# Kernel optimization log

Hardware: AMD Instinct MI355X
Metric: run time of the kernel (lower is better)

Reference implementation:

```python
import jax, jax.numpy as jnp
import numpy as np

IN_SZ = 256
OUT_SZ = 256
RANK = 60  # min(60, IN_SZ*OUT_SZ)
C = 512    # channel_size
N_SEL = 256
B = 1024


def setup_inputs() -> dict:
    key = jax.random.key(0)
    k_x, k_u, k_v, k_b, k_i = jax.random.split(key, 5)
    # match torch init scales: U ~ U(-sqrt(3/rank), ...), V ~ U(-sqrt(1/(in*out)),...)
    bu = np.sqrt(3.0 / RANK)
    bv = np.sqrt(1.0 / (IN_SZ * OUT_SZ))
    bb = np.sqrt(1.0 / RANK)
    x = jax.random.normal(k_x, (N_SEL, B, IN_SZ), dtype=jnp.float32)
    weights_U = jax.random.uniform(k_u, (C, RANK), jnp.float32, -bu, bu)
    weights_V = jax.random.uniform(k_v, (RANK, IN_SZ * OUT_SZ), jnp.float32, -bv, bv)
    bias = jax.random.uniform(k_b, (C, 1, OUT_SZ), jnp.float32, -bb, bb)
    indices = jax.random.randint(k_i, (N_SEL,), 0, C, dtype=jnp.int64)
    return {"x": x, "indices": indices, "weights_U": weights_U,
            "weights_V": weights_V, "bias": bias}


def reference(x, indices, weights_U, weights_V, bias):
    # Synthesize full per-channel weights, then gather selected channels
    # (faithful to the original: full U @ V materialized before gather).
    weight = (weights_U @ weights_V).reshape(-1, IN_SZ, OUT_SZ)  # [C, in, out]
    w = weight[indices]                                          # [n, in, out]
    # per-channel batched matmul: [n, B, in] x [n, in, out] -> [n, B, out]
    out = jnp.einsum('nbi,nio->nbo', x, w) + bias[indices]
    return out
```

## Files before the change

### kernel.cpp

```cpp
#include <hip/hip_runtime.h>
#include <hip/hip_bf16.h>
#include <stdint.h>

#define IN_SZ   256
#define OUT_SZ  256
#define RANK    60
#define NSEL    256
#define BATCH   1024
#define WELEMS  (IN_SZ * OUT_SZ)

typedef __attribute__((ext_vector_type(8))) short          short8;
typedef __attribute__((ext_vector_type(4))) float          f32x4;
typedef __attribute__((ext_vector_type(4))) unsigned short u16x4;

static __device__ __forceinline__ unsigned short f32_to_bf16(float f) {
    union { float f; uint32_t u; } c; c.f = f;
    uint32_t u = c.u;
    u += 0x7fffu + ((u >> 16) & 1u);
    return (unsigned short)(u >> 16);
}

__global__ __launch_bounds__(256) void synth_w(
    const float* __restrict__ U, const float* __restrict__ V,
    const int* __restrict__ idx, unsigned short* __restrict__ wt)
{
    __shared__ unsigned short Cs[16][2064];

    int bid = blockIdx.x;
    int L   = (bid & 7) * 64 + (bid >> 3);
    int ic  = L >> 4;
    int g16 = L & 15;

    int tid = threadIdx.x, lane = tid & 63, wv = tid >> 6;

    int arow = lane & 15;
    int c    = idx[g16 * 16 + arow];
    short8 afr[2];
    #pragma unroll
    for (int ks = 0; ks < 2; ++ks) {
        short8 h;
        #pragma unroll
        for (int j = 0; j < 8; ++j) {
            int r = ks * 32 + (lane >> 4) * 8 + j;
            float u = (r < RANK) ? U[c * RANK + r] : 0.f;
            h[j] = (short)f32_to_bf16(u);
        }
        afr[ks] = h;
    }

    const float* Vb = V + (size_t)ic * 2048;
    #pragma unroll 2
    for (int mt = 0; mt < 32; ++mt) {
        int mloc = (wv * 32 + mt) * 16 + (lane & 15);
        f32x4 acc = {};
        #pragma unroll
        for (int ks = 0; ks < 2; ++ks) {
            short8 b;
            #pragma unroll
            for (int j = 0; j < 8; ++j) {
                int r = ks * 32 + (lane >> 4) * 8 + j;
                float v = (r < RANK) ? Vb[(size_t)r * WELEMS + mloc] : 0.f;
                b[j] = (short)f32_to_bf16(v);
            }
            acc = __builtin_amdgcn_mfma_f32_16x16x32_bf16(afr[ks], b, acc, 0, 0, 0);
        }
        #pragma unroll
        for (int j = 0; j < 4; ++j) {
            int nl = (lane >> 4) * 4 + j;
            Cs[nl][wv * 512 + mt * 16 + (lane & 15)] = f32_to_bf16(acc[j]);
        }
    }
    __syncthreads();

    #pragma unroll
    for (int t0 = 0; t0 < 16; ++t0) {
        int t  = t0 * 256 + tid;
        int nl = t >> 8;
        int o  = t & 255;
        short8 h;
        #pragma unroll
        for (int il = 0; il < 8; ++il) h[il] = (short)Cs[nl][il * 256 + o];
        int n = g16 * 16 + nl;
        size_t base = (size_t)n * WELEMS + (size_t)ic * 2048 + (size_t)o * 8;
        *reinterpret_cast<short8*>(wt + base) = h;
    }
}

__global__ __launch_bounds__(256, 3) void gemm_k(
    const float* __restrict__ x, const int* __restrict__ idx,
    const unsigned short* __restrict__ wt, const float* __restrict__ bias,
    float* __restrict__ out)
{
    __shared__ __align__(16) unsigned short As[64 * 256];

    int bid = blockIdx.x;
    int L   = (bid & 7) * 512 + (bid >> 3);
    int n   = L >> 4;
    int mt  = L & 15;

    int tid  = threadIdx.x;
    int lane = tid & 63;
    int wv   = tid >> 6;
    int r16  = lane & 15;
    int q    = lane >> 4;

    const float*          xn = x  + (size_t)n * (BATCH * IN_SZ) + (size_t)mt * 64 * IN_SZ;
    const unsigned short* wb = wt + (size_t)n * WELEMS;

    #pragma unroll
    for (int p = 0; p < 8; ++p) {
        int id    = p * 256 + tid;
        int row   = id >> 5;
        int chunk = id & 31;
        const float* gp = xn + (size_t)row * IN_SZ + chunk * 8;
        float4 v0 = *reinterpret_cast<const float4*>(gp);
        float4 v1 = *reinterpret_cast<const float4*>(gp + 4);
        short8 h;
        h[0] = (short)f32_to_bf16(v0.x); h[1] = (short)f32_to_bf16(v0.y);
        h[2] = (short)f32_to_bf16(v0.z); h[3] = (short)f32_to_bf16(v0.w);
        h[4] = (short)f32_to_bf16(v1.x); h[5] = (short)f32_to_bf16(v1.y);
        h[6] = (short)f32_to_bf16(v1.z); h[7] = (short)f32_to_bf16(v1.w);
        int off = row * 512 + ((chunk * 16) ^ ((row & 7) << 4));
        *reinterpret_cast<short8*>(&As[off >> 1]) = h;
    }
    __syncthreads();

    f32x4 acc[4][4] = {};

    #pragma unroll
    for (int ks = 0; ks < 8; ++ks) {
        short8 af[4], bf[4];
        #pragma unroll
        for (int mf = 0; mf < 4; ++mf) {
            int row = mf * 16 + r16;
            int off = row * 512 + ((ks * 64 + q * 16) ^ ((row & 7) << 4));
            af[mf] = *reinterpret_cast<const short8*>(&As[off >> 1]);
        }
        #pragma unroll
        for (int nf = 0; nf < 4; ++nf) {
            int o = wv * 64 + nf * 16 + r16;
            bf[nf] = *reinterpret_cast<const short8*>(
                wb + (size_t)((ks * 4 + q) * 2048 + o * 8));
        }
        #pragma unroll
        for (int mf = 0; mf < 4; ++mf)
            #pragma unroll
            for (int nf = 0; nf < 4; ++nf)
                acc[mf][nf] = __builtin_amdgcn_mfma_f32_16x16x32_bf16(
                    af[mf], bf[nf], acc[mf][nf], 0, 0, 0);
    }

    int c = idx[n];
    float bv[4];
    #pragma unroll
    for (int nf = 0; nf < 4; ++nf)
        bv[nf] = bias[(size_t)c * OUT_SZ + wv * 64 + nf * 16 + r16];

    float* on = out + (size_t)n * (BATCH * OUT_SZ) + (size_t)mt * 64 * OUT_SZ;
    #pragma unroll
    for (int mf = 0; mf < 4; ++mf) {
        int r0 = mf * 16 + q * 4;
        #pragma unroll
        for (int nf = 0; nf < 4; ++nf) {
            int o = wv * 64 + nf * 16 + r16;
            #pragma unroll
            for (int j = 0; j < 4; ++j)
                on[(size_t)(r0 + j) * OUT_SZ + o] = acc[mf][nf][j] + bv[nf];
        }
    }
}

extern "C" void kernel_launch(void* const* d_in, const int* in_sizes, int n_in,
                              void* d_out, int out_size, void* d_ws, size_t ws_size,
                              hipStream_t stream) {
    const float* x    = (const float*)d_in[0];
    const int*   idx  = (const int*)  d_in[1];
    const float* U    = (const float*)d_in[2];
    const float* V    = (const float*)d_in[3];
    const float* bias = (const float*)d_in[4];
    float* out = (float*)d_out;
    unsigned short* wt = (unsigned short*)d_ws;
    (void)in_sizes; (void)n_in; (void)out_size; (void)ws_size;

    synth_w<<<dim3(512),  dim3(256), 0, stream>>>(U, V, idx, wt);
    gemm_k <<<dim3(4096), dim3(256), 0, stream>>>(x, idx, wt, bias, out);
}
```

Measured before the change: 171.4 us.

## Make gemm blocks loop over four M-tiles with prefetched x and B fragments

Each gemm block now handles four 64-row tiles of one channel instead of one, so grid shrinks from 4096 to 1024 blocks. The next x tile is loaded into registers during compute, B fragments are triple-buffered, and MFMA operands are swapped so outputs are stored as contiguous float4 with vector bias loads. This targets global latency stalls and scattered scalar stores. The cost is higher register pressure (occupancy hint lowered to 2) and fewer blocks to spread across CUs.

```diff
diff --git a/kernel.cpp b/kernel.cpp
--- a/kernel.cpp
+++ b/kernel.cpp
@@ -86,86 +86,117 @@
     }
 }
 
-__global__ __launch_bounds__(256, 3) void gemm_k(
+__global__ __launch_bounds__(256, 2) void gemm_k(
     const float* __restrict__ x, const int* __restrict__ idx,
     const unsigned short* __restrict__ wt, const float* __restrict__ bias,
     float* __restrict__ out)
 {
     __shared__ __align__(16) unsigned short As[64 * 256];
 
-    int bid = blockIdx.x;
-    int L   = (bid & 7) * 512 + (bid >> 3);
-    int n   = L >> 4;
-    int mt  = L & 15;
-
-    int tid  = threadIdx.x;
-    int lane = tid & 63;
-    int wv   = tid >> 6;
-    int r16  = lane & 15;
-    int q    = lane >> 4;
-
-    const float*          xn = x  + (size_t)n * (BATCH * IN_SZ) + (size_t)mt * 64 * IN_SZ;
+    int bid  = blockIdx.x;
+    int L    = (bid & 7) * 128 + (bid >> 3);
+    int n    = L >> 2;
+    int quad = L & 3;
+
+    int tid = threadIdx.x, lane = tid & 63, wv = tid >> 6;
+    int r16 = lane & 15, q = lane >> 4;
+    int srow = tid >> 5, schunk = tid & 31;
+
     const unsigned short* wb = wt + (size_t)n * WELEMS;
-
+    const float*          xb = x  + (size_t)n * (BATCH * IN_SZ);
+    float*                ob = out + (size_t)n * (BATCH * OUT_SZ);
+
+    int c = idx[n];
+    f32x4 bv4[4];
     #pragma unroll
-    for (int p = 0; p < 8; ++p) {
-        int id    = p * 256 + tid;
-        int row   = id >> 5;
-        int chunk = id & 31;
-        const float* gp = xn + (size_t)row * IN_SZ + chunk * 8;
-        float4 v0 = *reinterpret_cast<const float4*>(gp);
-        float4 v1 = *reinterpret_cast<const float4*>(gp + 4);
-        short8 h;
-        h[0] = (short)f32_to_bf16(v0.x); h[1] = (short)f32_to_bf16(v0.y);
-        h[2] = (short)f32_to_bf16(v0.z); h[3] = (short)f32_to_bf16(v0.w);
-        h[4] = (short)f32_to_bf16(v1.x); h[5] = (short)f32_to_bf16(v1.y);
-        h[6] = (short)f32_to_bf16(v1.z); h[7] = (short)f32_to_bf16(v1.w);
-        int off = row * 512 + ((chunk * 16) ^ ((row & 7) << 4));
-        *reinterpret_cast<short8*>(&As[off >> 1]) = h;
-    }
+    for (int nf = 0; nf < 4; ++nf)
+        bv4[nf] = *reinterpret_cast<const f32x4*>(
+            &bias[(size_t)c * OUT_SZ + wv * 64 + nf * 16 + q * 4]);
+
+    float4 va[8][2];
+
+    auto issue_x = [&](int mt) {
+        const float* xn = xb + (size_t)mt * 64 * IN_SZ;
+        #pragma unroll
+        for (int p = 0; p < 8; ++p) {
+            int row = p * 8 + srow;
+            const float* gp = xn + (size_t)row * IN_SZ + schunk * 8;
+            va[p][0] = *reinterpret_cast<const float4*>(gp);
+            va[p][1] = *reinterpret_cast<const float4*>(gp + 4);
+        }
+    };
+    auto write_lds = [&]() {
+        #pragma unroll
+        for (int p = 0; p < 8; ++p) {
+            int row = p * 8 + srow;
+            short8 h;
+            h[0] = (short)f32_to_bf16(va[p][0].x); h[1] = (short)f32_to_bf16(va[p][0].y);
+            h[2] = (short)f32_to_bf16(va[p][0].z); h[3] = (short)f32_to_bf16(va[p][0].w);
+            h[4] = (short)f32_to_bf16(va[p][1].x); h[5] = (short)f32_to_bf16(va[p][1].y);
+            h[6] = (short)f32_to_bf16(va[p][1].z); h[7] = (short)f32_to_bf16(va[p][1].w);
+            int off = row * 512 + ((schunk * 16) ^ ((row & 7) << 4));
+            *reinterpret_cast<short8*>(&As[off >> 1]) = h;
+        }
+    };
+
+    const unsigned short* wq = wb + q * 2048 + (size_t)(wv * 64 + r16) * 8;
+    auto loadB = [&](int ks, short8* dst) {
+        #pragma unroll
+        for (int nf = 0; nf < 4; ++nf)
+            dst[nf] = *reinterpret_cast<const short8*>(wq + ks * 8192 + nf * 128);
+    };
+
+    f32x4 acc[4][4] = {};
+    short8 bf[3][4];
+
+    loadB(0, bf[0]);
+    loadB(1, bf[1]);
+    issue_x(quad * 4);
+    write_lds();
     __syncthreads();
 
-    f32x4 acc[4][4] = {};
-
-    #pragma unroll
-    for (int ks = 0; ks < 8; ++ks) {
-        short8 af[4], bf[4];
+    for (int t = 0; t < 4; ++t) {
+        int mt = quad * 4 + t;
+
+        #pragma unroll
+        for (int ks = 0; ks < 8; ++ks) {
+            if (ks < 6) loadB(ks + 2, bf[(ks + 2) % 3]);
+            if (ks == 5 && t < 3) issue_x(mt + 1);
+            short8 af[4];
+            #pragma unroll
+            for (int mf = 0; mf < 4; ++mf) {
+                int row = mf * 16 + r16;
+                int off = row * 512 + ((ks * 64 + q * 16) ^ ((row & 7) << 4));
+                af[mf] = *reinterpret_cast<const short8*>(&As[off >> 1]);
+            }
+            const short8* bb = bf[ks % 3];
+            #pragma unroll
+            for (int mf = 0; mf < 4; ++mf)
+                #pragma unroll
+                for (int nf = 0; nf < 4; ++nf)
+                    acc[mf][nf] = __builtin_amdgcn_mfma_f32_16x16x32_bf16(
+                        bb[nf], af[mf], acc[mf][nf], 0, 0, 0);
+        }
+
+        if (t < 3) {
+            __syncthreads();
+            write_lds();
+            __syncthreads();
+            loadB(0, bf[0]);
+            loadB(1, bf[1]);
+        }
+
+        float* on = ob + (size_t)mt * 64 * OUT_SZ;
         #pragma unroll
         for (int mf = 0; mf < 4; ++mf) {
             int row = mf * 16 + r16;
-            int off = row * 512 + ((ks * 64 + q * 16) ^ ((row & 7) << 4));
-            af[mf] = *reinterpret_cast<const short8*>(&As[off >> 1]);
-        }
-        #pragma unroll
-        for (int nf = 0; nf < 4; ++nf) {
-            int o = wv * 64 + nf * 16 + r16;
-            bf[nf] = *reinterpret_cast<const short8*>(
-                wb + (size_t)((ks * 4 + q) * 2048 + o * 8));
-        }
-        #pragma unroll
-        for (int mf = 0; mf < 4; ++mf)
-            #pragma unroll
-            for (int nf = 0; nf < 4; ++nf)
-                acc[mf][nf] = __builtin_amdgcn_mfma_f32_16x16x32_bf16(
-                    af[mf], bf[nf], acc[mf][nf], 0, 0, 0);
-    }
-
-    int c = idx[n];
-    float bv[4];
-    #pragma unroll
-    for (int nf = 0; nf < 4; ++nf)
-        bv[nf] = bias[(size_t)c * OUT_SZ + wv * 64 + nf * 16 + r16];
-
-    float* on = out + (size_t)n * (BATCH * OUT_SZ) + (size_t)mt * 64 * OUT_SZ;
-    #pragma unroll
-    for (int mf = 0; mf < 4; ++mf) {
-        int r0 = mf * 16 + q * 4;
-        #pragma unroll
-        for (int nf = 0; nf < 4; ++nf) {
-            int o = wv * 64 + nf * 16 + r16;
-            #pragma unroll
-            for (int j = 0; j < 4; ++j)
-                on[(size_t)(r0 + j) * OUT_SZ + o] = acc[mf][nf][j] + bv[nf];
+            #pragma unroll
+            for (int nf = 0; nf < 4; ++nf) {
+                f32x4 w = acc[mf][nf] + bv4[nf];
+                *reinterpret_cast<f32x4*>(
+                    &on[(size_t)row * OUT_SZ + wv * 64 + nf * 16 + q * 4]) = w;
+                if (t < 3) acc[mf][nf] = (f32x4){0.f, 0.f, 0.f, 0.f};
+            }
         }
     }
 }
@@ -183,5 +214,5 @@
     (void)in_sizes; (void)n_in; (void)out_size; (void)ws_size;
 
     synth_w<<<dim3(512),  dim3(256), 0, stream>>>(U, V, idx, wt);
-    gemm_k <<<dim3(4096), dim3(256), 0, stream>>>(x, idx, wt, bias, out);
-}
+    gemm_k <<<dim3(1024), dim3(256), 0, stream>>>(x, idx, wt, bias, out);
+}
```

Measured after the change: 301.2 us. 1.76x slower.

## Pipeline x loads into LDS via direct global-to-LDS DMA with triple buffering

Applied to the files above, without the earlier changes.

The GEMM kernel stops loading the full 64x256 x tile into registers, converting to bf16 and storing it to LDS before any compute. Instead it streams fp32 x in four K-slices through a triple-buffered LDS ring using global_load_lds, with manual vmcnt waits and barriers, and converts to bf16 when the fragments are read. It also swaps the MFMA operand order so each lane holds four consecutive output columns, which lets the bias add and output store use 16-byte vector writes. This overlaps global load latency with MFMA work and cuts scalar stores, but it doubles LDS bytes per element (fp32) and moves the conversion cost into the inner loop.

```diff
diff --git a/kernel.cpp b/kernel.cpp
--- a/kernel.cpp
+++ b/kernel.cpp
@@ -11,7 +11,6 @@
 
 typedef __attribute__((ext_vector_type(8))) short          short8;
 typedef __attribute__((ext_vector_type(4))) float          f32x4;
-typedef __attribute__((ext_vector_type(4))) unsigned short u16x4;
 
 static __device__ __forceinline__ unsigned short f32_to_bf16(float f) {
     union { float f; uint32_t u; } c; c.f = f;
@@ -19,6 +18,18 @@
     u += 0x7fffu + ((u >> 16) & 1u);
     return (unsigned short)(u >> 16);
 }
+
+static __device__ __forceinline__ short8 cvt8(f32x4 lo, f32x4 hi) {
+    union { short8 s; __hip_bfloat162 h[4]; } u;
+    u.h[0] = __float22bfloat162_rn(make_float2(lo[0], lo[1]));
+    u.h[1] = __float22bfloat162_rn(make_float2(lo[2], lo[3]));
+    u.h[2] = __float22bfloat162_rn(make_float2(hi[0], hi[1]));
+    u.h[3] = __float22bfloat162_rn(make_float2(hi[2], hi[3]));
+    return u.s;
+}
+
+#define VM_WAIT4 asm volatile("s_waitcnt vmcnt(4)" ::: "memory")
+#define VM_WAIT0 asm volatile("s_waitcnt vmcnt(0)" ::: "memory")
 
 __global__ __launch_bounds__(256) void synth_w(
     const float* __restrict__ U, const float* __restrict__ V,
@@ -91,7 +102,7 @@
     const unsigned short* __restrict__ wt, const float* __restrict__ bias,
     float* __restrict__ out)
 {
-    __shared__ __align__(16) unsigned short As[64 * 256];
+    __shared__ __align__(16) float As[3][64 * 64];
 
     int bid = blockIdx.x;
     int L   = (bid & 7) * 512 + (bid >> 3);
@@ -105,67 +116,91 @@
     int q    = lane >> 4;
 
     const float*          xn = x  + (size_t)n * (BATCH * IN_SZ) + (size_t)mt * 64 * IN_SZ;
-    const unsigned short* wb = wt + (size_t)n * WELEMS;
-
-    #pragma unroll
-    for (int p = 0; p < 8; ++p) {
-        int id    = p * 256 + tid;
-        int row   = id >> 5;
-        int chunk = id & 31;
-        const float* gp = xn + (size_t)row * IN_SZ + chunk * 8;
-        float4 v0 = *reinterpret_cast<const float4*>(gp);
-        float4 v1 = *reinterpret_cast<const float4*>(gp + 4);
-        short8 h;
-        h[0] = (short)f32_to_bf16(v0.x); h[1] = (short)f32_to_bf16(v0.y);
-        h[2] = (short)f32_to_bf16(v0.z); h[3] = (short)f32_to_bf16(v0.w);
-        h[4] = (short)f32_to_bf16(v1.x); h[5] = (short)f32_to_bf16(v1.y);
-        h[6] = (short)f32_to_bf16(v1.z); h[7] = (short)f32_to_bf16(v1.w);
-        int off = row * 512 + ((chunk * 16) ^ ((row & 7) << 4));
-        *reinterpret_cast<short8*>(&As[off >> 1]) = h;
-    }
-    __syncthreads();
+    const unsigned short* wq = wt + (size_t)n * WELEMS + q * 2048
+                                  + (size_t)(wv * 64 + r16) * 8;
+
+    auto dma = [&](int b, int kt) {
+        #pragma unroll
+        for (int p = 0; p < 4; ++p) {
+            int id  = p * 256 + tid;
+            int row = id >> 4;
+            int sc  = (id & 15) ^ (row & 7);
+            const float* gp = xn + (size_t)row * IN_SZ + kt * 64 + sc * 4;
+            int base = ((p * 256 + wv * 64) >> 4) * 64;
+            __builtin_amdgcn_global_load_lds(
+                (const __attribute__((address_space(1))) void*)gp,
+                (__attribute__((address_space(3))) void*)(&As[b][base]),
+                16, 0, 0);
+        }
+    };
+    auto loadB = [&](int kt, short8 bf[2][4]) {
+        #pragma unroll
+        for (int kk = 0; kk < 2; ++kk)
+            #pragma unroll
+            for (int nf = 0; nf < 4; ++nf)
+                bf[kk][nf] = *reinterpret_cast<const short8*>(
+                    wq + (size_t)kt * 16384 + kk * 8192 + nf * 128);
+    };
 
     f32x4 acc[4][4] = {};
 
-    #pragma unroll
-    for (int ks = 0; ks < 8; ++ks) {
-        short8 af[4], bf[4];
-        #pragma unroll
-        for (int mf = 0; mf < 4; ++mf) {
-            int row = mf * 16 + r16;
-            int off = row * 512 + ((ks * 64 + q * 16) ^ ((row & 7) << 4));
-            af[mf] = *reinterpret_cast<const short8*>(&As[off >> 1]);
-        }
-        #pragma unroll
-        for (int nf = 0; nf < 4; ++nf) {
-            int o = wv * 64 + nf * 16 + r16;
-            bf[nf] = *reinterpret_cast<const short8*>(
-                wb + (size_t)((ks * 4 + q) * 2048 + o * 8));
-        }
-        #pragma unroll
-        for (int mf = 0; mf < 4; ++mf)
-            #pragma unroll
-            for (int nf = 0; nf < 4; ++nf)
-                acc[mf][nf] = __builtin_amdgcn_mfma_f32_16x16x32_bf16(
-                    af[mf], bf[nf], acc[mf][nf], 0, 0, 0);
-    }
+    auto computeT = [&](int b, short8 bf[2][4]) {
+        #pragma unroll
+        for (int kk = 0; kk < 2; ++kk) {
+            short8 af[4];
+            #pragma unroll
+            for (int mf = 0; mf < 4; ++mf) {
+                int row = mf * 16 + r16;
+                int s   = row & 7;
+                int c0  = kk * 8 + q * 2;
+                f32x4 lo = *reinterpret_cast<const f32x4*>(
+                    &As[b][row * 64 + ((c0 ^ s) << 2)]);
+                f32x4 hi = *reinterpret_cast<const f32x4*>(
+                    &As[b][row * 64 + (((c0 + 1) ^ s) << 2)]);
+                af[mf] = cvt8(lo, hi);
+            }
+            #pragma unroll
+            for (int mf = 0; mf < 4; ++mf)
+                #pragma unroll
+                for (int nf = 0; nf < 4; ++nf)
+                    acc[mf][nf] = __builtin_amdgcn_mfma_f32_16x16x32_bf16(
+                        bf[kk][nf], af[mf], acc[mf][nf], 0, 0, 0);
+        }
+    };
+
+    short8 bf[2][4];
+
+    dma(0, 0);
+    dma(1, 1);
+    VM_WAIT4; __builtin_amdgcn_s_barrier(); __builtin_amdgcn_sched_barrier(0);
+
+    loadB(0, bf); dma(2, 2);
+    computeT(0, bf);
+    VM_WAIT4; __builtin_amdgcn_s_barrier(); __builtin_amdgcn_sched_barrier(0);
+
+    loadB(1, bf); dma(0, 3);
+    computeT(1, bf);
+    VM_WAIT4; __builtin_amdgcn_s_barrier(); __builtin_amdgcn_sched_barrier(0);
+
+    loadB(2, bf);
+    computeT(2, bf);
+    VM_WAIT0; __builtin_amdgcn_s_barrier(); __builtin_amdgcn_sched_barrier(0);
+
+    loadB(3, bf);
+    computeT(0 + 0, bf);
+    ;
 
     int c = idx[n];
-    float bv[4];
-    #pragma unroll
-    for (int nf = 0; nf < 4; ++nf)
-        bv[nf] = bias[(size_t)c * OUT_SZ + wv * 64 + nf * 16 + r16];
-
     float* on = out + (size_t)n * (BATCH * OUT_SZ) + (size_t)mt * 64 * OUT_SZ;
     #pragma unroll
-    for (int mf = 0; mf < 4; ++mf) {
-        int r0 = mf * 16 + q * 4;
-        #pragma unroll
-        for (int nf = 0; nf < 4; ++nf) {
-            int o = wv * 64 + nf * 16 + r16;
-            #pragma unroll
-            for (int j = 0; j < 4; ++j)
-                on[(size_t)(r0 + j) * OUT_SZ + o] = acc[mf][nf][j] + bv[nf];
+    for (int nf = 0; nf < 4; ++nf) {
+        f32x4 bv = *reinterpret_cast<const f32x4*>(
+            &bias[(size_t)c * OUT_SZ + wv * 64 + nf * 16 + q * 4]);
+        #pragma unroll
+        for (int mf = 0; mf < 4; ++mf) {
+            f32x4 w = acc[mf][nf] + bv;
+            *reinterpret_cast<f32x4*>(
+                &on[(size_t)(mf * 16 + r16) * OUT_SZ + wv * 64 + nf * 16 + q * 4]) = w;
         }
     }
 }
```

Result: no change. 173.1 us (+1.0%).
